# Kernel optimization log

Hardware: AMD Instinct MI355X
Metric: run time of the kernel (lower is better)

## Reference

```python
import jax, jax.numpy as jnp
import numpy as np

DIM = 256
HEADS = 8
WS = 8
SHIFT = 0
MLP_HIDDEN = 1024
N = 16
HH = 64
WW = 64
EPS = 1e-6


def _rel_pos_index(ws):
    # same construction as the torch buffer
    coords = np.stack(np.meshgrid(np.arange(ws), np.arange(ws), indexing='ij'))  # [2,ws,ws]
    cf = coords.reshape(2, -1)  # [2, T]
    rel = cf[:, :, None] - cf[:, None, :]  # [2,T,T]
    rel = rel.transpose(1, 2, 0).copy()
    rel[:, :, 0] += ws - 1
    rel[:, :, 1] += ws - 1
    rel[:, :, 0] *= 2 * ws - 1
    return rel.sum(-1)  # [T,T] int


REL_IDX = jnp.asarray(_rel_pos_index(WS), dtype=jnp.int32)


def setup_inputs() -> dict:
    key = jax.random.key(0)
    ks = jax.random.split(key, 12)
    s = 0.02
    return {
        'x_seq': jax.random.normal(ks[0], (N, HH * WW, DIM), jnp.float32),
        'c': jax.random.normal(ks[1], (N, DIM), jnp.float32),
        'qkv_w': jax.random.normal(ks[2], (DIM, 3 * DIM), jnp.float32) * s,
        'qkv_b': jnp.zeros((3 * DIM,), jnp.float32),
        'proj_w': jax.random.normal(ks[3], (DIM, DIM), jnp.float32) * s,
        'proj_b': jnp.zeros((DIM,), jnp.float32),
        'rel_pos_bias': jax.random.normal(ks[4], ((2 * WS - 1) ** 2, HEADS), jnp.float32) * s,
        'ada_w': jax.random.normal(ks[5], (DIM, 6 * DIM), jnp.float32) * s,
        'ada_b': jnp.zeros((6 * DIM,), jnp.float32),
        'fc1_w': jax.random.normal(ks[6], (DIM, MLP_HIDDEN), jnp.float32) * s,
        'fc1_b': jnp.zeros((MLP_HIDDEN,), jnp.float32),
        'fc2_w': jax.random.normal(ks[7], (MLP_HIDDEN, DIM), jnp.float32) * s,
        'fc2_b': jnp.zeros((DIM,), jnp.float32),
        'H': HH,
        'W': WW,
    }


def _ln(x):
    mu = jnp.mean(x, axis=-1, keepdims=True)
    var = jnp.mean(jnp.square(x - mu), axis=-1, keepdims=True)
    return (x - mu) / jnp.sqrt(var + EPS)


def _modulate(x, shift, scale):
    return x * (1.0 + scale[:, None, :]) + shift[:, None, :]


def _window_attention(x, qkv_w, qkv_b, proj_w, proj_b, rel_pos_bias):
    B_, T, C = x.shape
    hd = C // HEADS
    qkv = (x @ qkv_w + qkv_b).reshape(B_, T, 3, HEADS, hd)
    q = qkv[:, :, 0].transpose(0, 2, 1, 3) * (hd ** -0.5)  # [B_,h,T,d]
    k = qkv[:, :, 1].transpose(0, 2, 1, 3)
    v = qkv[:, :, 2].transpose(0, 2, 1, 3)
    attn = jnp.einsum('bhtd,bhsd->bhts', q, k)
    bias = rel_pos_bias[REL_IDX.reshape(-1)].reshape(T, T, HEADS).transpose(2, 0, 1)  # [h,T,T]
    attn = jax.nn.softmax(attn + bias[None], axis=-1)
    out = jnp.einsum('bhts,bhsd->bhtd', attn, v)
    out = out.transpose(0, 2, 1, 3).reshape(B_, T, C)
    return out @ proj_w + proj_b


def reference(x_seq, c, qkv_w, qkv_b, proj_w, proj_b, rel_pos_bias,
              ada_w, ada_b, fc1_w, fc1_b, fc2_w, fc2_b, H, W):
    Nb, T, C = x_seq.shape
    ws = WS
    ada = jax.nn.silu(c) @ ada_w + ada_b  # [N, 6C]
    sh_msa, sc_msa, g_msa, sh_mlp, sc_mlp, g_mlp = jnp.split(ada, 6, axis=1)

    x = x_seq.reshape(Nb, H, W, C)
    pad_h = (ws - H % ws) % ws
    pad_w = (ws - W % ws) % ws
    if pad_h or pad_w:
        x = jnp.pad(x, ((0, 0), (0, pad_h), (0, pad_w), (0, 0)))
    Hp, Wp = x.shape[1], x.shape[2]
    if SHIFT > 0:
        x = jnp.roll(x, shift=(-SHIFT, -SHIFT), axis=(1, 2))

    # window partition: [N*nW, ws*ws, C]
    x_win = x.reshape(Nb, Hp // ws, ws, Wp // ws, ws, C).transpose(0, 1, 3, 2, 4, 5)
    x_win = x_win.reshape(-1, ws * ws, C)
    nW = (Hp // ws) * (Wp // ws)

    sh_w = jnp.repeat(sh_msa, nW, axis=0)
    sc_w = jnp.repeat(sc_msa, nW, axis=0)
    g_w = jnp.repeat(g_msa, nW, axis=0)

    h = _modulate(_ln(x_win), sh_w, sc_w)
    h = _window_attention(h, qkv_w, qkv_b, proj_w, proj_b, rel_pos_bias)
    x_win = x_win + g_w[:, None, :] * h

    # window unpartition
    x = x_win.reshape(Nb, Hp // ws, Wp // ws, ws, ws, C).transpose(0, 1, 3, 2, 4, 5)
    x = x.reshape(Nb, Hp, Wp, C)
    if SHIFT > 0:
        x = jnp.roll(x, shift=(SHIFT, SHIFT), axis=(1, 2))
    if pad_h or pad_w:
        x = x[:, :H, :W, :]
    x = x.reshape(Nb, T, C)

    h = _modulate(_ln(x), sh_mlp, sc_mlp)
    h = jax.nn.gelu(h @ fc1_w + fc1_b, approximate=True) @ fc2_w + fc2_b
    return x + g_mlp[:, None, :] * h
```

## Files before the change

kernel.cpp:

```cpp
#include <hip/hip_runtime.h>
#include <hip/hip_bf16.h>

#define TTOT 65536

using f32x4 = __attribute__((ext_vector_type(4))) float;
using s16x8 = __attribute__((ext_vector_type(8))) short;
typedef unsigned short u16;
using u16x8 = __attribute__((ext_vector_type(8))) u16;

__device__ __forceinline__ u16 f2bf(float f) {
    return __bfloat16_as_ushort(__float2bfloat16(f));
}

__global__ void wconv_t(const float* __restrict__ w, __hip_bfloat16* __restrict__ wt,
                        int K, int N) {
    int idx = blockIdx.x * 256 + threadIdx.x;
    if (idx >= K * N) return;
    int n = idx / K, k = idx - n * K;
    wt[idx] = __float2bfloat16(w[(long)k * N + n]);
}

__global__ __launch_bounds__(256) void ada_kernel(const float* __restrict__ c,
                                                  const float* __restrict__ ada_w,
                                                  const float* __restrict__ ada_b,
                                                  float* __restrict__ ada) {
    __shared__ float sc[16 * 256];
    int tid = threadIdx.x;
    for (int i = tid; i < 16 * 256; i += 256) {
        float v = c[i];
        sc[i] = v / (1.0f + expf(-v));
    }
    __syncthreads();
    int j = blockIdx.x * 256 + tid;
    float b = ada_b[j];
    for (int n = 0; n < 16; n++) {
        float acc = b;
        for (int k = 0; k < 256; k++)
            acc += sc[n * 256 + k] * ada_w[(long)k * 1536 + j];
        ada[n * 1536 + j] = acc;
    }
}

__global__ __launch_bounds__(512) void attn_mega(const float* __restrict__ x_seq,
                                                 const __hip_bfloat16* __restrict__ qkvw,
                                                 const float* __restrict__ qkv_b,
                                                 const __hip_bfloat16* __restrict__ projw,
                                                 const float* __restrict__ proj_b,
                                                 const float* __restrict__ rpb,
                                                 const float* __restrict__ ada,
                                                 float* __restrict__ outf) {
    __shared__ u16 xa[64 * 264];
    __shared__ u16 qk[2 * 64 * 264];
    __shared__ u16 vt[8][32 * 72];
    __shared__ float bs[8 * 225];

    int tid = threadIdx.x;
    int lane = tid & 63;
    int h = tid >> 6;
    int la = lane & 15, lb = lane >> 4;
    int win = blockIdx.x;
    int n = win >> 6, wh = (win >> 3) & 7, ww = win & 7;
    long base = (long)n * 4096 + (long)(wh * 8) * 64 + ww * 8;

    for (int i = tid; i < 1800; i += 512) bs[i] = rpb[(i % 225) * 8 + (i / 225)];

    {
        const float* shp = &ada[n * 1536 + 0];
        const float* scp = &ada[n * 1536 + 256];
#pragma unroll
        for (int i = 0; i < 8; i++) {
            int t = h * 8 + i;
            long sr = base + h * 64 + i;
            const float4 v = *(const float4*)&x_seq[sr * 256 + lane * 4];
            float s = v.x + v.y + v.z + v.w;
            float s2 = v.x * v.x + v.y * v.y + v.z * v.z + v.w * v.w;
#pragma unroll
            for (int o = 32; o > 0; o >>= 1) {
                s += __shfl_xor(s, o, 64);
                s2 += __shfl_xor(s2, o, 64);
            }
            float mu = s * (1.0f / 256.0f);
            float var = s2 * (1.0f / 256.0f) - mu * mu;
            float rstd = rsqrtf(var + 1e-6f);
            float vv[4] = {v.x, v.y, v.z, v.w};
#pragma unroll
            for (int e = 0; e < 4; e++) {
                int col = lane * 4 + e;
                float val = (vv[e] - mu) * rstd;
                xa[t * 264 + col] = f2bf(val * (1.0f + scp[col]) + shp[col]);
            }
        }
    }
    __syncthreads();

    const u16* W = (const u16*)qkvw;

#pragma unroll
    for (int m = 0; m < 3; m++) {
        const u16* Wm = W + (long)(m * 256 + h * 32) * 256;
        float bb0 = qkv_b[m * 256 + h * 32 + la];
        float bb1 = qkv_b[m * 256 + h * 32 + 16 + la];
        s16x8 bfr[2][8];
#pragma unroll
        for (int ct = 0; ct < 2; ct++)
#pragma unroll
            for (int kc = 0; kc < 8; kc++)
                bfr[ct][kc] = *(const s16x8*)&Wm[(ct * 16 + la) * 256 + kc * 32 + lb * 8];
        f32x4 acc[4][2] = {};
#pragma unroll
        for (int kc = 0; kc < 8; kc++) {
            s16x8 a[4];
#pragma unroll
            for (int rt = 0; rt < 4; rt++)
                a[rt] = *(const s16x8*)&xa[(rt * 16 + la) * 264 + kc * 32 + lb * 8];
#pragma unroll
            for (int rt = 0; rt < 4; rt++)
#pragma unroll
                for (int ct = 0; ct < 2; ct++)
                    acc[rt][ct] = __builtin_amdgcn_mfma_f32_16x16x32_bf16(
                        a[rt], bfr[ct][kc], acc[rt][ct], 0, 0, 0);
        }
        if (m < 2) {
            u16* dst = &qk[m * 16896];
#pragma unroll
            for (int rt = 0; rt < 4; rt++)
#pragma unroll
                for (int ct = 0; ct < 2; ct++)
#pragma unroll
                    for (int r = 0; r < 4; r++)
                        dst[(rt * 16 + lb * 4 + r) * 264 + h * 32 + ct * 16 + la] =
                            f2bf(acc[rt][ct][r] + (ct ? bb1 : bb0));
        } else {
#pragma unroll
            for (int rt = 0; rt < 4; rt++)
#pragma unroll
                for (int ct = 0; ct < 2; ct++)
#pragma unroll
                    for (int r = 0; r < 4; r++)
                        vt[h][(ct * 16 + la) * 72 + rt * 16 + lb * 4 + r] =
                            f2bf(acc[rt][ct][r] + (ct ? bb1 : bb0));
        }
    }
    __syncthreads();

    s16x8 qf[4], kf[4];
#pragma unroll
    for (int rt = 0; rt < 4; rt++) {
        qf[rt] = *(const s16x8*)&qk[(rt * 16 + la) * 264 + h * 32 + lb * 8];
        kf[rt] = *(const s16x8*)&qk[16896 + (rt * 16 + la) * 264 + h * 32 + lb * 8];
    }
    f32x4 sa[4][4];
    f32x4 zero = {};
#pragma unroll
    for (int rt = 0; rt < 4; rt++)
#pragma unroll
        for (int ct = 0; ct < 4; ct++)
            sa[rt][ct] = __builtin_amdgcn_mfma_f32_16x16x32_bf16(qf[rt], kf[ct], zero, 0, 0, 0);

    float rls[4][4];
    int jr = (la >> 3);
    int jc = la & 7;
#pragma unroll
    for (int rt = 0; rt < 4; rt++) {
#pragma unroll
        for (int r = 0; r < 4; r++) {
            int t = rt * 16 + lb * 4 + r;
            int tr = t >> 3, tc = t & 7;
            const float* bh = &bs[h * 225 + (tr + 7) * 15 + (tc - jc + 7)];
            float v0 = sa[rt][0][r] * 0.17677669529663687f + bh[-(0 * 2 + jr) * 15];
            float v1 = sa[rt][1][r] * 0.17677669529663687f + bh[-(1 * 2 + jr) * 15];
            float v2 = sa[rt][2][r] * 0.17677669529663687f + bh[-(2 * 2 + jr) * 15];
            float v3 = sa[rt][3][r] * 0.17677669529663687f + bh[-(3 * 2 + jr) * 15];
            float mx = fmaxf(fmaxf(v0, v1), fmaxf(v2, v3));
#pragma unroll
            for (int o = 1; o < 16; o <<= 1) mx = fmaxf(mx, __shfl_xor(mx, o, 64));
            float p0 = __expf(v0 - mx), p1 = __expf(v1 - mx);
            float p2 = __expf(v2 - mx), p3 = __expf(v3 - mx);
            float sum = (p0 + p1) + (p2 + p3);
#pragma unroll
            for (int o = 1; o < 16; o <<= 1) sum += __shfl_xor(sum, o, 64);
            sa[rt][0][r] = p0; sa[rt][1][r] = p1; sa[rt][2][r] = p2; sa[rt][3][r] = p3;
            rls[rt][r] = 1.0f / sum;
        }
    }
    __syncthreads();

    u16* P = &qk[h * 4096];
#pragma unroll
    for (int rt = 0; rt < 4; rt++)
#pragma unroll
        for (int ct = 0; ct < 4; ct++)
#pragma unroll
            for (int r = 0; r < 4; r++) {
                int t = rt * 16 + lb * 4 + r;
                int slot = ct * 2 + (la >> 3);
                P[t * 64 + ((slot ^ (t & 7)) << 3) + (la & 7)] = f2bf(sa[rt][ct][r]);
            }
    __syncthreads();

    f32x4 oa[4][2] = {};
#pragma unroll
    for (int ks = 0; ks < 2; ks++) {
        s16x8 vf[2];
#pragma unroll
        for (int dt = 0; dt < 2; dt++)
            vf[dt] = *(const s16x8*)&vt[h][(dt * 16 + la) * 72 + ks * 32 + lb * 8];
#pragma unroll
        for (int rt = 0; rt < 4; rt++) {
            int t = rt * 16 + la;
            s16x8 pf = *(const s16x8*)&P[t * 64 + (((ks * 4 + lb) ^ (t & 7)) << 3)];
#pragma unroll
            for (int dt = 0; dt < 2; dt++)
                oa[rt][dt] = __builtin_amdgcn_mfma_f32_16x16x32_bf16(pf, vf[dt], oa[rt][dt], 0, 0, 0);
        }
    }
#pragma unroll
    for (int rt = 0; rt < 4; rt++)
#pragma unroll
        for (int dt = 0; dt < 2; dt++)
#pragma unroll
            for (int r = 0; r < 4; r++)
                xa[(rt * 16 + lb * 4 + r) * 264 + h * 32 + dt * 16 + la] =
                    f2bf(oa[rt][dt][r] * rls[rt][r]);
    __syncthreads();

    {
        const u16* Pw = (const u16*)projw + (long)(h * 32) * 256;
        s16x8 bfr[2][8];
#pragma unroll
        for (int ct = 0; ct < 2; ct++)
#pragma unroll
            for (int kc = 0; kc < 8; kc++)
                bfr[ct][kc] = *(const s16x8*)&Pw[(ct * 16 + la) * 256 + kc * 32 + lb * 8];
        f32x4 pj[4][2] = {};
#pragma unroll
        for (int kc = 0; kc < 8; kc++) {
            s16x8 a[4];
#pragma unroll
            for (int rt = 0; rt < 4; rt++)
                a[rt] = *(const s16x8*)&xa[(rt * 16 + la) * 264 + kc * 32 + lb * 8];
#pragma unroll
            for (int rt = 0; rt < 4; rt++)
#pragma unroll
                for (int ct = 0; ct < 2; ct++)
                    pj[rt][ct] = __builtin_amdgcn_mfma_f32_16x16x32_bf16(
                        a[rt], bfr[ct][kc], pj[rt][ct], 0, 0, 0);
        }
        float g0 = ada[n * 1536 + 512 + h * 32 + la];
        float g1 = ada[n * 1536 + 512 + h * 32 + 16 + la];
        float pb0 = proj_b[h * 32 + la];
        float pb1 = proj_b[h * 32 + 16 + la];
#pragma unroll
        for (int rt = 0; rt < 4; rt++) {
#pragma unroll
            for (int r = 0; r < 4; r++) {
                int t = rt * 16 + lb * 4 + r;
                long sr = base + (t >> 3) * 64 + (t & 7);
#pragma unroll
                for (int ct = 0; ct < 2; ct++) {
                    int col = h * 32 + ct * 16 + la;
                    float v = pj[rt][ct][r] + (ct ? pb1 : pb0);
                    outf[sr * 256 + col] = x_seq[sr * 256 + col] + (ct ? g1 : g0) * v;
                }
            }
        }
    }
}

__global__ __launch_bounds__(256, 2) void mlp_fused(float* __restrict__ outf,
                                                    const __hip_bfloat16* __restrict__ fc1w,
                                                    const float* __restrict__ fc1_b,
                                                    const __hip_bfloat16* __restrict__ fc2w,
                                                    const float* __restrict__ fc2_b,
                                                    const float* __restrict__ ada) {
    __shared__ u16 xa[64 * 264];
    __shared__ u16 hb[64 * 268];

    int tid = threadIdx.x;
    int lane = tid & 63;
    int w = tid >> 6;
    int la = lane & 15, lb = lane >> 4;
    long mrow = (long)blockIdx.x * 64;
    int nb = (int)(mrow >> 12);

    const u16* F1 = (const u16*)fc1w;
    const u16* F2 = (const u16*)fc2w;

    const float* sh = &ada[nb * 1536 + 768];
    const float* scp = &ada[nb * 1536 + 1024];
#pragma unroll
    for (int i = 0; i < 16; i++) {
        int row = i * 4 + w;
        const float4 v = *(const float4*)&outf[(mrow + row) * 256 + lane * 4];
        float s = v.x + v.y + v.z + v.w;
        float s2 = v.x * v.x + v.y * v.y + v.z * v.z + v.w * v.w;
#pragma unroll
        for (int o = 32; o > 0; o >>= 1) {
            s += __shfl_xor(s, o, 64);
            s2 += __shfl_xor(s2, o, 64);
        }
        float mu = s * (1.0f / 256.0f);
        float var = s2 * (1.0f / 256.0f) - mu * mu;
        float rstd = rsqrtf(var + 1e-6f);
        float vv[4] = {v.x, v.y, v.z, v.w};
#pragma unroll
        for (int e = 0; e < 4; e++) {
            int col = lane * 4 + e;
            float val = (vv[e] - mu) * rstd;
            val = val * (1.0f + scp[col]) + sh[col];
            xa[row * 264 + col] = f2bf(val);
        }
    }
    __syncthreads();

    f32x4 acc2[4][4] = {};

#pragma unroll 1
    for (int c = 0; c < 4; c++) {
        f32x4 acc1[4][4] = {};
        const u16* B1 = F1 + (long)(c * 256 + w * 64) * 256;
        s16x8 bc[8];
#pragma unroll
        for (int ct = 0; ct < 4; ct++)
#pragma unroll
            for (int kk = 0; kk < 2; kk++)
                bc[ct * 2 + kk] = *(const s16x8*)&B1[(ct * 16 + la) * 256 + kk * 32 + lb * 8];
#pragma unroll
        for (int k0 = 0; k0 < 4; k0++) {
            s16x8 bn[8];
            if (k0 < 3) {
#pragma unroll
                for (int ct = 0; ct < 4; ct++)
#pragma unroll
                    for (int kk = 0; kk < 2; kk++)
                        bn[ct * 2 + kk] = *(const s16x8*)&B1[(ct * 16 + la) * 256 +
                                                             (k0 + 1) * 64 + kk * 32 + lb * 8];
            }
            s16x8 a[4][2];
#pragma unroll
            for (int rt = 0; rt < 4; rt++)
#pragma unroll
                for (int kk = 0; kk < 2; kk++)
                    a[rt][kk] = *(const s16x8*)&xa[(rt * 16 + la) * 264 +
                                                   k0 * 64 + kk * 32 + lb * 8];
            __builtin_amdgcn_s_setprio(1);
#pragma unroll
            for (int kk = 0; kk < 2; kk++)
#pragma unroll
                for (int rt = 0; rt < 4; rt++)
#pragma unroll
                    for (int ct = 0; ct < 4; ct++)
                        acc1[rt][ct] = __builtin_amdgcn_mfma_f32_16x16x32_bf16(
                            a[rt][kk], bc[ct * 2 + kk], acc1[rt][ct], 0, 0, 0);
            __builtin_amdgcn_s_setprio(0);
            if (k0 < 3) {
#pragma unroll
                for (int q = 0; q < 8; q++) bc[q] = bn[q];
            }
        }
#pragma unroll
        for (int ct = 0; ct < 4; ct++) {
            float b1v = fc1_b[c * 256 + w * 64 + ct * 16 + la];
#pragma unroll
            for (int rt = 0; rt < 4; rt++) {
#pragma unroll
                for (int r = 0; r < 4; r++) {
                    float v = acc1[rt][ct][r] + b1v;
                    float u2 = 1.5957691216057308f * (v + 0.044715f * v * v * v);
                    hb[(rt * 16 + lb * 4 + r) * 268 + w * 64 + ct * 16 + la] =
                        f2bf(v / (1.0f + __expf(-u2)));
                }
            }
        }
        __syncthreads();

        const u16* B2 = F2 + (long)(w * 64) * 1024 + c * 256;
        s16x8 bc2[8];
#pragma unroll
        for (int ct = 0; ct < 4; ct++)
#pragma unroll
            for (int kk = 0; kk < 2; kk++)
                bc2[ct * 2 + kk] = *(const s16x8*)&B2[(ct * 16 + la) * 1024 + kk * 32 + lb * 8];
#pragma unroll
        for (int k0 = 0; k0 < 4; k0++) {
            s16x8 bn2[8];
            if (k0 < 3) {
#pragma unroll
                for (int ct = 0; ct < 4; ct++)
#pragma unroll
                    for (int kk = 0; kk < 2; kk++)
                        bn2[ct * 2 + kk] = *(const s16x8*)&B2[(ct * 16 + la) * 1024 +
                                                              (k0 + 1) * 64 + kk * 32 + lb * 8];
            }
            s16x8 a[4][2];
#pragma unroll
            for (int rt = 0; rt < 4; rt++)
#pragma unroll
                for (int kk = 0; kk < 2; kk++)
                    a[rt][kk] = *(const s16x8*)&hb[(rt * 16 + la) * 268 +
                                                   k0 * 64 + kk * 32 + lb * 8];
            __builtin_amdgcn_s_setprio(1);
#pragma unroll
            for (int kk = 0; kk < 2; kk++)
#pragma unroll
                for (int rt = 0; rt < 4; rt++)
#pragma unroll
                    for (int ct = 0; ct < 4; ct++)
                        acc2[rt][ct] = __builtin_amdgcn_mfma_f32_16x16x32_bf16(
                            a[rt][kk], bc2[ct * 2 + kk], acc2[rt][ct], 0, 0, 0);
            __builtin_amdgcn_s_setprio(0);
            if (k0 < 3) {
#pragma unroll
                for (int q = 0; q < 8; q++) bc2[q] = bn2[q];
            }
        }
        __syncthreads();
    }

#pragma unroll
    for (int ct = 0; ct < 4; ct++) {
        int col = w * 64 + ct * 16 + la;
        float g = ada[nb * 1536 + 1280 + col];
        float b2v = fc2_b[col];
#pragma unroll
        for (int rt = 0; rt < 4; rt++) {
#pragma unroll
            for (int r = 0; r < 4; r++) {
                long row = mrow + rt * 16 + lb * 4 + r;
                long oidx = row * 256 + col;
                outf[oidx] = outf[oidx] + g * (acc2[rt][ct][r] + b2v);
            }
        }
    }
}

extern "C" void kernel_launch(void* const* d_in, const int* in_sizes, int n_in,
                              void* d_out, int out_size, void* d_ws, size_t ws_size,
                              hipStream_t stream) {
    const float* x_seq  = (const float*)d_in[0];
    const float* c      = (const float*)d_in[1];
    const float* qkv_w  = (const float*)d_in[2];
    const float* qkv_b  = (const float*)d_in[3];
    const float* proj_w = (const float*)d_in[4];
    const float* proj_b = (const float*)d_in[5];
    const float* rpb    = (const float*)d_in[6];
    const float* ada_w  = (const float*)d_in[7];
    const float* ada_b  = (const float*)d_in[8];
    const float* fc1_w  = (const float*)d_in[9];
    const float* fc1_b  = (const float*)d_in[10];
    const float* fc2_w  = (const float*)d_in[11];
    const float* fc2_b  = (const float*)d_in[12];

    char* ws = (char*)d_ws;
    float* ada             = (float*)ws;
    __hip_bfloat16* qkv_wt = (__hip_bfloat16*)(ws + 131072);
    __hip_bfloat16* proj_wt= (__hip_bfloat16*)(ws + 524288);
    __hip_bfloat16* fc1_wt = (__hip_bfloat16*)(ws + 655360);
    __hip_bfloat16* fc2_wt = (__hip_bfloat16*)(ws + 1179648);
    float* outf = (float*)d_out;

    wconv_t<<<(256 * 768 + 255) / 256, 256, 0, stream>>>(qkv_w, qkv_wt, 256, 768);
    wconv_t<<<(256 * 256 + 255) / 256, 256, 0, stream>>>(proj_w, proj_wt, 256, 256);
    wconv_t<<<(256 * 1024 + 255) / 256, 256, 0, stream>>>(fc1_w, fc1_wt, 256, 1024);
    wconv_t<<<(1024 * 256 + 255) / 256, 256, 0, stream>>>(fc2_w, fc2_wt, 1024, 256);

    ada_kernel<<<6, 256, 0, stream>>>(c, ada_w, ada_b, ada);

    attn_mega<<<1024, 512, 0, stream>>>(x_seq, qkv_wt, qkv_b, proj_wt, proj_b,
                                        rpb, ada, outf);

    mlp_fused<<<TTOT / 64, 256, 0, stream>>>(outf, fc1_wt, fc1_b, fc2_wt, fc2_b, ada);
}
```

Before: 361.2 us.

## Split attention rows across two waves per head with 1024-thread blocks

```diff
diff --git a/kernel.cpp b/kernel.cpp
--- a/kernel.cpp
+++ b/kernel.cpp
@@ -41,14 +41,14 @@
     }
 }
 
-__global__ __launch_bounds__(512) void attn_mega(const float* __restrict__ x_seq,
-                                                 const __hip_bfloat16* __restrict__ qkvw,
-                                                 const float* __restrict__ qkv_b,
-                                                 const __hip_bfloat16* __restrict__ projw,
-                                                 const float* __restrict__ proj_b,
-                                                 const float* __restrict__ rpb,
-                                                 const float* __restrict__ ada,
-                                                 float* __restrict__ outf) {
+__global__ __launch_bounds__(1024) void attn_mega(const float* __restrict__ x_seq,
+                                                  const __hip_bfloat16* __restrict__ qkvw,
+                                                  const float* __restrict__ qkv_b,
+                                                  const __hip_bfloat16* __restrict__ projw,
+                                                  const float* __restrict__ proj_b,
+                                                  const float* __restrict__ rpb,
+                                                  const float* __restrict__ ada,
+                                                  float* __restrict__ outf) {
     __shared__ u16 xa[64 * 264];
     __shared__ u16 qk[2 * 64 * 264];
     __shared__ u16 vt[8][32 * 72];
@@ -56,30 +56,32 @@
 
     int tid = threadIdx.x;
     int lane = tid & 63;
-    int h = tid >> 6;
+    int wv = tid >> 6;
+    int h = wv >> 1;
+    int s = wv & 1;
     int la = lane & 15, lb = lane >> 4;
     int win = blockIdx.x;
     int n = win >> 6, wh = (win >> 3) & 7, ww = win & 7;
     long base = (long)n * 4096 + (long)(wh * 8) * 64 + ww * 8;
 
-    for (int i = tid; i < 1800; i += 512) bs[i] = rpb[(i % 225) * 8 + (i / 225)];
+    for (int i = tid; i < 1800; i += 1024) bs[i] = rpb[(i % 225) * 8 + (i / 225)];
 
     {
         const float* shp = &ada[n * 1536 + 0];
         const float* scp = &ada[n * 1536 + 256];
 #pragma unroll
-        for (int i = 0; i < 8; i++) {
-            int t = h * 8 + i;
-            long sr = base + h * 64 + i;
+        for (int i = 0; i < 4; i++) {
+            int t = wv * 4 + i;
+            long sr = base + (t >> 3) * 64 + (t & 7);
             const float4 v = *(const float4*)&x_seq[sr * 256 + lane * 4];
-            float s = v.x + v.y + v.z + v.w;
+            float ssum = v.x + v.y + v.z + v.w;
             float s2 = v.x * v.x + v.y * v.y + v.z * v.z + v.w * v.w;
 #pragma unroll
             for (int o = 32; o > 0; o >>= 1) {
-                s += __shfl_xor(s, o, 64);
+                ssum += __shfl_xor(ssum, o, 64);
                 s2 += __shfl_xor(s2, o, 64);
             }
-            float mu = s * (1.0f / 256.0f);
+            float mu = ssum * (1.0f / 256.0f);
             float var = s2 * (1.0f / 256.0f) - mu * mu;
             float rstd = rsqrtf(var + 1e-6f);
             float vv[4] = {v.x, v.y, v.z, v.w};
@@ -106,71 +108,72 @@
 #pragma unroll
             for (int kc = 0; kc < 8; kc++)
                 bfr[ct][kc] = *(const s16x8*)&Wm[(ct * 16 + la) * 256 + kc * 32 + lb * 8];
-        f32x4 acc[4][2] = {};
+        f32x4 acc[2][2] = {};
 #pragma unroll
         for (int kc = 0; kc < 8; kc++) {
-            s16x8 a[4];
-#pragma unroll
-            for (int rt = 0; rt < 4; rt++)
-                a[rt] = *(const s16x8*)&xa[(rt * 16 + la) * 264 + kc * 32 + lb * 8];
-#pragma unroll
-            for (int rt = 0; rt < 4; rt++)
+            s16x8 a[2];
+#pragma unroll
+            for (int q = 0; q < 2; q++)
+                a[q] = *(const s16x8*)&xa[((s * 2 + q) * 16 + la) * 264 + kc * 32 + lb * 8];
+#pragma unroll
+            for (int q = 0; q < 2; q++)
 #pragma unroll
                 for (int ct = 0; ct < 2; ct++)
-                    acc[rt][ct] = __builtin_amdgcn_mfma_f32_16x16x32_bf16(
-                        a[rt], bfr[ct][kc], acc[rt][ct], 0, 0, 0);
+                    acc[q][ct] = __builtin_amdgcn_mfma_f32_16x16x32_bf16(
+                        a[q], bfr[ct][kc], acc[q][ct], 0, 0, 0);
         }
         if (m < 2) {
             u16* dst = &qk[m * 16896];
 #pragma unroll
-            for (int rt = 0; rt < 4; rt++)
+            for (int q = 0; q < 2; q++)
 #pragma unroll
                 for (int ct = 0; ct < 2; ct++)
 #pragma unroll
                     for (int r = 0; r < 4; r++)
-                        dst[(rt * 16 + lb * 4 + r) * 264 + h * 32 + ct * 16 + la] =
-                            f2bf(acc[rt][ct][r] + (ct ? bb1 : bb0));
+                        dst[((s * 2 + q) * 16 + lb * 4 + r) * 264 + h * 32 + ct * 16 + la] =
+                            f2bf(acc[q][ct][r] + (ct ? bb1 : bb0));
         } else {
 #pragma unroll
-            for (int rt = 0; rt < 4; rt++)
+            for (int q = 0; q < 2; q++)
 #pragma unroll
                 for (int ct = 0; ct < 2; ct++)
 #pragma unroll
                     for (int r = 0; r < 4; r++)
-                        vt[h][(ct * 16 + la) * 72 + rt * 16 + lb * 4 + r] =
-                            f2bf(acc[rt][ct][r] + (ct ? bb1 : bb0));
-        }
-    }
-    __syncthreads();
-
-    s16x8 qf[4], kf[4];
-#pragma unroll
-    for (int rt = 0; rt < 4; rt++) {
-        qf[rt] = *(const s16x8*)&qk[(rt * 16 + la) * 264 + h * 32 + lb * 8];
-        kf[rt] = *(const s16x8*)&qk[16896 + (rt * 16 + la) * 264 + h * 32 + lb * 8];
-    }
-    f32x4 sa[4][4];
+                        vt[h][(ct * 16 + la) * 72 + (s * 2 + q) * 16 + lb * 4 + r] =
+                            f2bf(acc[q][ct][r] + (ct ? bb1 : bb0));
+        }
+    }
+    __syncthreads();
+
+    s16x8 qf[2], kf[4];
+#pragma unroll
+    for (int q = 0; q < 2; q++)
+        qf[q] = *(const s16x8*)&qk[((s * 2 + q) * 16 + la) * 264 + h * 32 + lb * 8];
+#pragma unroll
+    for (int ct = 0; ct < 4; ct++)
+        kf[ct] = *(const s16x8*)&qk[16896 + (ct * 16 + la) * 264 + h * 32 + lb * 8];
+    f32x4 sa[2][4];
     f32x4 zero = {};
 #pragma unroll
-    for (int rt = 0; rt < 4; rt++)
+    for (int q = 0; q < 2; q++)
 #pragma unroll
         for (int ct = 0; ct < 4; ct++)
-            sa[rt][ct] = __builtin_amdgcn_mfma_f32_16x16x32_bf16(qf[rt], kf[ct], zero, 0, 0, 0);
-
-    float rls[4][4];
+            sa[q][ct] = __builtin_amdgcn_mfma_f32_16x16x32_bf16(qf[q], kf[ct], zero, 0, 0, 0);
+
+    float rls[2][4];
     int jr = (la >> 3);
     int jc = la & 7;
 #pragma unroll
-    for (int rt = 0; rt < 4; rt++) {
+    for (int q = 0; q < 2; q++) {
 #pragma unroll
         for (int r = 0; r < 4; r++) {
-            int t = rt * 16 + lb * 4 + r;
+            int t = (s * 2 + q) * 16 + lb * 4 + r;
             int tr = t >> 3, tc = t & 7;
             const float* bh = &bs[h * 225 + (tr + 7) * 15 + (tc - jc + 7)];
-            float v0 = sa[rt][0][r] * 0.17677669529663687f + bh[-(0 * 2 + jr) * 15];
-            float v1 = sa[rt][1][r] * 0.17677669529663687f + bh[-(1 * 2 + jr) * 15];
-            float v2 = sa[rt][2][r] * 0.17677669529663687f + bh[-(2 * 2 + jr) * 15];
-            float v3 = sa[rt][3][r] * 0.17677669529663687f + bh[-(3 * 2 + jr) * 15];
+            float v0 = sa[q][0][r] * 0.17677669529663687f + bh[-(0 * 2 + jr) * 15];
+            float v1 = sa[q][1][r] * 0.17677669529663687f + bh[-(1 * 2 + jr) * 15];
+            float v2 = sa[q][2][r] * 0.17677669529663687f + bh[-(2 * 2 + jr) * 15];
+            float v3 = sa[q][3][r] * 0.17677669529663687f + bh[-(3 * 2 + jr) * 15];
             float mx = fmaxf(fmaxf(v0, v1), fmaxf(v2, v3));
 #pragma unroll
             for (int o = 1; o < 16; o <<= 1) mx = fmaxf(mx, __shfl_xor(mx, o, 64));
@@ -179,26 +182,26 @@
             float sum = (p0 + p1) + (p2 + p3);
 #pragma unroll
             for (int o = 1; o < 16; o <<= 1) sum += __shfl_xor(sum, o, 64);
-            sa[rt][0][r] = p0; sa[rt][1][r] = p1; sa[rt][2][r] = p2; sa[rt][3][r] = p3;
-            rls[rt][r] = 1.0f / sum;
+            sa[q][0][r] = p0; sa[q][1][r] = p1; sa[q][2][r] = p2; sa[q][3][r] = p3;
+            rls[q][r] = 1.0f / sum;
         }
     }
     __syncthreads();
 
     u16* P = &qk[h * 4096];
 #pragma unroll
-    for (int rt = 0; rt < 4; rt++)
+    for (int q = 0; q < 2; q++)
 #pragma unroll
         for (int ct = 0; ct < 4; ct++)
 #pragma unroll
             for (int r = 0; r < 4; r++) {
-                int t = rt * 16 + lb * 4 + r;
+                int t = (s * 2 + q) * 16 + lb * 4 + r;
                 int slot = ct * 2 + (la >> 3);
-                P[t * 64 + ((slot ^ (t & 7)) << 3) + (la & 7)] = f2bf(sa[rt][ct][r]);
-            }
-    __syncthreads();
-
-    f32x4 oa[4][2] = {};
+                P[t * 64 + ((slot ^ (t & 7)) << 3) + (la & 7)] = f2bf(sa[q][ct][r]);
+            }
+    __syncthreads();
+
+    f32x4 oa[2][2] = {};
 #pragma unroll
     for (int ks = 0; ks < 2; ks++) {
         s16x8 vf[2];
@@ -206,22 +209,22 @@
         for (int dt = 0; dt < 2; dt++)
             vf[dt] = *(const s16x8*)&vt[h][(dt * 16 + la) * 72 + ks * 32 + lb * 8];
 #pragma unroll
-        for (int rt = 0; rt < 4; rt++) {
-            int t = rt * 16 + la;
+        for (int q = 0; q < 2; q++) {
+            int t = (s * 2 + q) * 16 + la;
             s16x8 pf = *(const s16x8*)&P[t * 64 + (((ks * 4 + lb) ^ (t & 7)) << 3)];
 #pragma unroll
             for (int dt = 0; dt < 2; dt++)
-                oa[rt][dt] = __builtin_amdgcn_mfma_f32_16x16x32_bf16(pf, vf[dt], oa[rt][dt], 0, 0, 0);
-        }
-    }
-#pragma unroll
-    for (int rt = 0; rt < 4; rt++)
+                oa[q][dt] = __builtin_amdgcn_mfma_f32_16x16x32_bf16(pf, vf[dt], oa[q][dt], 0, 0, 0);
+        }
+    }
+#pragma unroll
+    for (int q = 0; q < 2; q++)
 #pragma unroll
         for (int dt = 0; dt < 2; dt++)
 #pragma unroll
             for (int r = 0; r < 4; r++)
-                xa[(rt * 16 + lb * 4 + r) * 264 + h * 32 + dt * 16 + la] =
-                    f2bf(oa[rt][dt][r] * rls[rt][r]);
+                xa[((s * 2 + q) * 16 + lb * 4 + r) * 264 + h * 32 + dt * 16 + la] =
+                    f2bf(oa[q][dt][r] * rls[q][r]);
     __syncthreads();
 
     {
@@ -232,34 +235,34 @@
 #pragma unroll
             for (int kc = 0; kc < 8; kc++)
                 bfr[ct][kc] = *(const s16x8*)&Pw[(ct * 16 + la) * 256 + kc * 32 + lb * 8];
-        f32x4 pj[4][2] = {};
+        f32x4 pj[2][2] = {};
 #pragma unroll
         for (int kc = 0; kc < 8; kc++) {
-            s16x8 a[4];
-#pragma unroll
-            for (int rt = 0; rt < 4; rt++)
-                a[rt] = *(const s16x8*)&xa[(rt * 16 + la) * 264 + kc * 32 + lb * 8];
-#pragma unroll
-            for (int rt = 0; rt < 4; rt++)
+            s16x8 a[2];
+#pragma unroll
+            for (int q = 0; q < 2; q++)
+                a[q] = *(const s16x8*)&xa[((s * 2 + q) * 16 + la) * 264 + kc * 32 + lb * 8];
+#pragma unroll
+            for (int q = 0; q < 2; q++)
 #pragma unroll
                 for (int ct = 0; ct < 2; ct++)
-                    pj[rt][ct] = __builtin_amdgcn_mfma_f32_16x16x32_bf16(
-                        a[rt], bfr[ct][kc], pj[rt][ct], 0, 0, 0);
+                    pj[q][ct] = __builtin_amdgcn_mfma_f32_16x16x32_bf16(
+                        a[q], bfr[ct][kc], pj[q][ct], 0, 0, 0);
         }
         float g0 = ada[n * 1536 + 512 + h * 32 + la];
         float g1 = ada[n * 1536 + 512 + h * 32 + 16 + la];
         float pb0 = proj_b[h * 32 + la];
         float pb1 = proj_b[h * 32 + 16 + la];
 #pragma unroll
-        for (int rt = 0; rt < 4; rt++) {
+        for (int q = 0; q < 2; q++) {
 #pragma unroll
             for (int r = 0; r < 4; r++) {
-                int t = rt * 16 + lb * 4 + r;
+                int t = (s * 2 + q) * 16 + lb * 4 + r;
                 long sr = base + (t >> 3) * 64 + (t & 7);
 #pragma unroll
                 for (int ct = 0; ct < 2; ct++) {
                     int col = h * 32 + ct * 16 + la;
-                    float v = pj[rt][ct][r] + (ct ? pb1 : pb0);
+                    float v = pj[q][ct][r] + (ct ? pb1 : pb0);
                     outf[sr * 256 + col] = x_seq[sr * 256 + col] + (ct ? g1 : g0) * v;
                 }
             }
@@ -466,8 +469,8 @@
 
     ada_kernel<<<6, 256, 0, stream>>>(c, ada_w, ada_b, ada);
 
-    attn_mega<<<1024, 512, 0, stream>>>(x_seq, qkv_wt, qkv_b, proj_wt, proj_b,
-                                        rpb, ada, outf);
+    attn_mega<<<1024, 1024, 0, stream>>>(x_seq, qkv_wt, qkv_b, proj_wt, proj_b,
+                                         rpb, ada, outf);
 
     mlp_fused<<<TTOT / 64, 256, 0, stream>>>(outf, fc1_wt, fc1_b, fc2_wt, fc2_b, ada);
 }
```

Measured after the change: 422.2 us. 1.17x slower.

## Fuse MLP into attention kernel per window, keeping residual in shared memory

Applied to the files above, without the earlier changes.

```diff
diff --git a/kernel.cpp b/kernel.cpp
--- a/kernel.cpp
+++ b/kernel.cpp
@@ -1,12 +1,9 @@
 #include <hip/hip_runtime.h>
 #include <hip/hip_bf16.h>
-
-#define TTOT 65536
 
 using f32x4 = __attribute__((ext_vector_type(4))) float;
 using s16x8 = __attribute__((ext_vector_type(8))) short;
 typedef unsigned short u16;
-using u16x8 = __attribute__((ext_vector_type(8))) u16;
 
 __device__ __forceinline__ u16 f2bf(float f) {
     return __bfloat16_as_ushort(__float2bfloat16(f));
@@ -41,13 +38,17 @@
     }
 }
 
-__global__ __launch_bounds__(512) void attn_mega(const float* __restrict__ x_seq,
+__global__ __launch_bounds__(512) void swin_mega(const float* __restrict__ x_seq,
                                                  const __hip_bfloat16* __restrict__ qkvw,
                                                  const float* __restrict__ qkv_b,
                                                  const __hip_bfloat16* __restrict__ projw,
                                                  const float* __restrict__ proj_b,
                                                  const float* __restrict__ rpb,
                                                  const float* __restrict__ ada,
+                                                 const __hip_bfloat16* __restrict__ fc1w,
+                                                 const float* __restrict__ fc1_b,
+                                                 const __hip_bfloat16* __restrict__ fc2w,
+                                                 const float* __restrict__ fc2_b,
                                                  float* __restrict__ outf) {
     __shared__ u16 xa[64 * 264];
     __shared__ u16 qk[2 * 64 * 264];
@@ -56,7 +57,8 @@
 
     int tid = threadIdx.x;
     int lane = tid & 63;
-    int h = tid >> 6;
+    int wv = tid >> 6;
+    int h = wv;
     int la = lane & 15, lb = lane >> 4;
     int win = blockIdx.x;
     int n = win >> 6, wh = (win >> 3) & 7, ww = win & 7;
@@ -224,6 +226,8 @@
                     f2bf(oa[rt][dt][r] * rls[rt][r]);
     __syncthreads();
 
+    float* o1 = (float*)qk;
+
     {
         const u16* Pw = (const u16*)projw + (long)(h * 32) * 256;
         s16x8 bfr[2][8];
@@ -260,65 +264,53 @@
                 for (int ct = 0; ct < 2; ct++) {
                     int col = h * 32 + ct * 16 + la;
                     float v = pj[rt][ct][r] + (ct ? pb1 : pb0);
-                    outf[sr * 256 + col] = x_seq[sr * 256 + col] + (ct ? g1 : g0) * v;
+                    o1[t * 260 + col] = x_seq[sr * 256 + col] + (ct ? g1 : g0) * v;
                 }
             }
         }
     }
-}
-
-__global__ __launch_bounds__(256, 2) void mlp_fused(float* __restrict__ outf,
-                                                    const __hip_bfloat16* __restrict__ fc1w,
-                                                    const float* __restrict__ fc1_b,
-                                                    const __hip_bfloat16* __restrict__ fc2w,
-                                                    const float* __restrict__ fc2_b,
-                                                    const float* __restrict__ ada) {
-    __shared__ u16 xa[64 * 264];
-    __shared__ u16 hb[64 * 268];
-
-    int tid = threadIdx.x;
-    int lane = tid & 63;
-    int w = tid >> 6;
-    int la = lane & 15, lb = lane >> 4;
-    long mrow = (long)blockIdx.x * 64;
-    int nb = (int)(mrow >> 12);
-
+    __syncthreads();
+
+    {
+        const float* shp = &ada[n * 1536 + 768];
+        const float* scp = &ada[n * 1536 + 1024];
+#pragma unroll
+        for (int i = 0; i < 8; i++) {
+            int t = wv * 8 + i;
+            const float4 v = *(const float4*)&o1[t * 260 + lane * 4];
+            float s = v.x + v.y + v.z + v.w;
+            float s2 = v.x * v.x + v.y * v.y + v.z * v.z + v.w * v.w;
+#pragma unroll
+            for (int o = 32; o > 0; o >>= 1) {
+                s += __shfl_xor(s, o, 64);
+                s2 += __shfl_xor(s2, o, 64);
+            }
+            float mu = s * (1.0f / 256.0f);
+            float var = s2 * (1.0f / 256.0f) - mu * mu;
+            float rstd = rsqrtf(var + 1e-6f);
+            float vv[4] = {v.x, v.y, v.z, v.w};
+#pragma unroll
+            for (int e = 0; e < 4; e++) {
+                int col = lane * 4 + e;
+                float val = (vv[e] - mu) * rstd;
+                xa[t * 264 + col] = f2bf(val * (1.0f + scp[col]) + shp[col]);
+            }
+        }
+    }
+    __syncthreads();
+
+    int s2 = wv >> 2;
+    int w2 = wv & 3;
+    u16* hb = (u16*)vt;
     const u16* F1 = (const u16*)fc1w;
     const u16* F2 = (const u16*)fc2w;
 
-    const float* sh = &ada[nb * 1536 + 768];
-    const float* scp = &ada[nb * 1536 + 1024];
-#pragma unroll
-    for (int i = 0; i < 16; i++) {
-        int row = i * 4 + w;
-        const float4 v = *(const float4*)&outf[(mrow + row) * 256 + lane * 4];
-        float s = v.x + v.y + v.z + v.w;
-        float s2 = v.x * v.x + v.y * v.y + v.z * v.z + v.w * v.w;
-#pragma unroll
-        for (int o = 32; o > 0; o >>= 1) {
-            s += __shfl_xor(s, o, 64);
-            s2 += __shfl_xor(s2, o, 64);
-        }
-        float mu = s * (1.0f / 256.0f);
-        float var = s2 * (1.0f / 256.0f) - mu * mu;
-        float rstd = rsqrtf(var + 1e-6f);
-        float vv[4] = {v.x, v.y, v.z, v.w};
-#pragma unroll
-        for (int e = 0; e < 4; e++) {
-            int col = lane * 4 + e;
-            float val = (vv[e] - mu) * rstd;
-            val = val * (1.0f + scp[col]) + sh[col];
-            xa[row * 264 + col] = f2bf(val);
-        }
-    }
-    __syncthreads();
-
-    f32x4 acc2[4][4] = {};
+    f32x4 acc2[2][4] = {};
 
 #pragma unroll 1
     for (int c = 0; c < 4; c++) {
-        f32x4 acc1[4][4] = {};
-        const u16* B1 = F1 + (long)(c * 256 + w * 64) * 256;
+        f32x4 acc1[2][4] = {};
+        const u16* B1 = F1 + (long)(c * 256 + w2 * 64) * 256;
         s16x8 bc[8];
 #pragma unroll
         for (int ct = 0; ct < 4; ct++)
@@ -336,45 +328,45 @@
                         bn[ct * 2 + kk] = *(const s16x8*)&B1[(ct * 16 + la) * 256 +
                                                              (k0 + 1) * 64 + kk * 32 + lb * 8];
             }
-            s16x8 a[4][2];
-#pragma unroll
-            for (int rt = 0; rt < 4; rt++)
+            s16x8 a[2][2];
+#pragma unroll
+            for (int q = 0; q < 2; q++)
 #pragma unroll
                 for (int kk = 0; kk < 2; kk++)
-                    a[rt][kk] = *(const s16x8*)&xa[(rt * 16 + la) * 264 +
-                                                   k0 * 64 + kk * 32 + lb * 8];
+                    a[q][kk] = *(const s16x8*)&xa[((s2 * 2 + q) * 16 + la) * 264 +
+                                                  k0 * 64 + kk * 32 + lb * 8];
             __builtin_amdgcn_s_setprio(1);
 #pragma unroll
             for (int kk = 0; kk < 2; kk++)
 #pragma unroll
-                for (int rt = 0; rt < 4; rt++)
+                for (int q = 0; q < 2; q++)
 #pragma unroll
                     for (int ct = 0; ct < 4; ct++)
-                        acc1[rt][ct] = __builtin_amdgcn_mfma_f32_16x16x32_bf16(
-                            a[rt][kk], bc[ct * 2 + kk], acc1[rt][ct], 0, 0, 0);
+                        acc1[q][ct] = __builtin_amdgcn_mfma_f32_16x16x32_bf16(
+                            a[q][kk], bc[ct * 2 + kk], acc1[q][ct], 0, 0, 0);
             __builtin_amdgcn_s_setprio(0);
             if (k0 < 3) {
 #pragma unroll
-                for (int q = 0; q < 8; q++) bc[q] = bn[q];
+                for (int q2 = 0; q2 < 8; q2++) bc[q2] = bn[q2];
             }
         }
 #pragma unroll
         for (int ct = 0; ct < 4; ct++) {
-            float b1v = fc1_b[c * 256 + w * 64 + ct * 16 + la];
-#pragma unroll
-            for (int rt = 0; rt < 4; rt++) {
+            float b1v = fc1_b[c * 256 + w2 * 64 + ct * 16 + la];
+#pragma unroll
+            for (int q = 0; q < 2; q++) {
 #pragma unroll
                 for (int r = 0; r < 4; r++) {
-                    float v = acc1[rt][ct][r] + b1v;
+                    float v = acc1[q][ct][r] + b1v;
                     float u2 = 1.5957691216057308f * (v + 0.044715f * v * v * v);
-                    hb[(rt * 16 + lb * 4 + r) * 268 + w * 64 + ct * 16 + la] =
+                    hb[((s2 * 2 + q) * 16 + lb * 4 + r) * 268 + w2 * 64 + ct * 16 + la] =
                         f2bf(v / (1.0f + __expf(-u2)));
                 }
             }
         }
         __syncthreads();
 
-        const u16* B2 = F2 + (long)(w * 64) * 1024 + c * 256;
+        const u16* B2 = F2 + (long)(w2 * 64) * 1024 + c * 256;
         s16x8 bc2[8];
 #pragma unroll
         for (int ct = 0; ct < 4; ct++)
@@ -392,26 +384,26 @@
                         bn2[ct * 2 + kk] = *(const s16x8*)&B2[(ct * 16 + la) * 1024 +
                                                               (k0 + 1) * 64 + kk * 32 + lb * 8];
             }
-            s16x8 a[4][2];
-#pragma unroll
-            for (int rt = 0; rt < 4; rt++)
+            s16x8 a[2][2];
+#pragma unroll
+            for (int q = 0; q < 2; q++)
 #pragma unroll
                 for (int kk = 0; kk < 2; kk++)
-                    a[rt][kk] = *(const s16x8*)&hb[(rt * 16 + la) * 268 +
-                                                   k0 * 64 + kk * 32 + lb * 8];
+                    a[q][kk] = *(const s16x8*)&hb[((s2 * 2 + q) * 16 + la) * 268 +
+                                                  k0 * 64 + kk * 32 + lb * 8];
             __builtin_amdgcn_s_setprio(1);
 #pragma unroll
             for (int kk = 0; kk < 2; kk++)
 #pragma unroll
-                for (int rt = 0; rt < 4; rt++)
+                for (int q = 0; q < 2; q++)
 #pragma unroll
                     for (int ct = 0; ct < 4; ct++)
-                        acc2[rt][ct] = __builtin_amdgcn_mfma_f32_16x16x32_bf16(
-                            a[rt][kk], bc2[ct * 2 + kk], acc2[rt][ct], 0, 0, 0);
+                        acc2[q][ct] = __builtin_amdgcn_mfma_f32_16x16x32_bf16(
+                            a[q][kk], bc2[ct * 2 + kk], acc2[q][ct], 0, 0, 0);
             __builtin_amdgcn_s_setprio(0);
             if (k0 < 3) {
 #pragma unroll
-                for (int q = 0; q < 8; q++) bc2[q] = bn2[q];
+                for (int q2 = 0; q2 < 8; q2++) bc2[q2] = bn2[q2];
             }
         }
         __syncthreads();
@@ -419,16 +411,16 @@
 
 #pragma unroll
     for (int ct = 0; ct < 4; ct++) {
-        int col = w * 64 + ct * 16 + la;
-        float g = ada[nb * 1536 + 1280 + col];
+        int col = w2 * 64 + ct * 16 + la;
+        float g = ada[n * 1536 + 1280 + col];
         float b2v = fc2_b[col];
 #pragma unroll
-        for (int rt = 0; rt < 4; rt++) {
+        for (int q = 0; q < 2; q++) {
 #pragma unroll
             for (int r = 0; r < 4; r++) {
-                long row = mrow + rt * 16 + lb * 4 + r;
-                long oidx = row * 256 + col;
-                outf[oidx] = outf[oidx] + g * (acc2[rt][ct][r] + b2v);
+                int t = (s2 * 2 + q) * 16 + lb * 4 + r;
+                long sr = base + (t >> 3) * 64 + (t & 7);
+                outf[sr * 256 + col] = o1[t * 260 + col] + g * (acc2[q][ct][r] + b2v);
             }
         }
     }
@@ -466,8 +458,7 @@
 
     ada_kernel<<<6, 256, 0, stream>>>(c, ada_w, ada_b, ada);
 
-    attn_mega<<<1024, 512, 0, stream>>>(x_seq, qkv_wt, qkv_b, proj_wt, proj_b,
-                                        rpb, ada, outf);
-
-    mlp_fused<<<TTOT / 64, 256, 0, stream>>>(outf, fc1_wt, fc1_b, fc2_wt, fc2_b, ada);
+    swin_mega<<<1024, 512, 0, stream>>>(x_seq, qkv_wt, qkv_b, proj_wt, proj_b,
+                                        rpb, ada, fc1_wt, fc1_b, fc2_wt, fc2_b,
+                                        outf);
 }
```

New measurement: 478.1 us. 1.32x slower.
